# Performance work log

Measured on AMD Instinct MI355X. Metric: run time of the kernel, lower is better.

Reference implementation:

```python
import jax, jax.numpy as jnp
import numpy as np

B, N, C, H = 2, 2048, 1024, 16
D = C // H
SCALE = D ** -0.5


def setup_inputs() -> dict:
    key = jax.random.key(0)
    ks = jax.random.split(key, 5)
    x = jax.random.normal(ks[0], (B, N, C), dtype=jnp.float32)
    # causal mask, broadcast over batch: True = attend
    attention_mask = jnp.broadcast_to(jnp.tril(jnp.ones((N, N), dtype=bool)), (B, N, N))
    w_qkv = jax.random.normal(ks[1], (3 * C, C), dtype=jnp.float32) * (C ** -0.5)
    b_qkv = jax.random.normal(ks[2], (3 * C,), dtype=jnp.float32) * 0.02
    w_proj = jax.random.normal(ks[3], (C, C), dtype=jnp.float32) * (C ** -0.5)
    b_proj = jax.random.normal(ks[4], (C,), dtype=jnp.float32) * 0.02
    return {"x": x, "attention_mask": attention_mask, "w_qkv": w_qkv,
            "b_qkv": b_qkv, "w_proj": w_proj, "b_proj": b_proj}


def reference(x, attention_mask, w_qkv, b_qkv, w_proj, b_proj):
    b, n, c = x.shape
    qkv = x @ w_qkv.T + b_qkv                      # [B,N,3C]
    qkv = qkv.reshape(b, n, 3, H, D).transpose(2, 0, 3, 1, 4)  # [3,B,H,N,D]
    q, k, v = qkv[0], qkv[1], qkv[2]
    dots = jnp.einsum('bhid,bhjd->bhij', q, k) * SCALE
    mask_value = -jnp.finfo(dots.dtype).max
    dots = jnp.where(attention_mask[:, None, :, :], dots, mask_value)
    attn = jax.nn.softmax(dots.astype(jnp.float32), axis=-1).astype(dots.dtype)
    out = jnp.einsum('bhij,bhjd->bhid', attn, v)   # [B,H,N,D]
    # NOTE: original code reshapes WITHOUT transposing heads back - faithful.
    out = out.reshape(b, n, c)
    return out @ w_proj.T + b_proj
```

## Files before the change

kernel.cpp:

```cpp
#include <hip/hip_runtime.h>
#include <hip/hip_bf16.h>
#include <stdint.h>

#define SL_F 0.18033688011112043f

typedef unsigned short u16;
typedef unsigned int u32;
typedef __attribute__((ext_vector_type(8))) short bf16x8;
typedef __attribute__((ext_vector_type(4))) float f32x4;

__device__ __forceinline__ u16 f2bf(float f) {
    union { float f; u32 u; } v; v.f = f;
    return (u16)((v.u + 0x7fffu + ((v.u >> 16) & 1u)) >> 16);
}
__device__ __forceinline__ u32 pack2bf(float a, float b) {
    union { __hip_bfloat162 h; u32 u; } p;
    p.h = __float22bfloat162_rn(make_float2(a, b));
    return p.u;
}

__device__ __forceinline__ void gl_lds16(const u16* g, u16* l) {
    __builtin_amdgcn_global_load_lds(
        (const __attribute__((address_space(1))) u32*)g,
        (__attribute__((address_space(3))) u32*)l, 16, 0, 0);
}

__global__ __launch_bounds__(256) void convert_k(
    const float4* __restrict__ x, const float4* __restrict__ w1,
    const float4* __restrict__ w2,
    ushort4* __restrict__ xb, ushort4* __restrict__ w1b, ushort4* __restrict__ w2b)
{
    const int i = blockIdx.x * 256 + threadIdx.x;
    const int XN = 4096 * 1024 / 4, W1 = 3072 * 1024 / 4;
    float4 v; ushort4* dst;
    if (i < XN)            { v = x[i];            dst = &xb[i]; }
    else if (i < XN + W1)  { v = w1[i - XN];      dst = &w1b[i - XN]; }
    else                   { v = w2[i - XN - W1]; dst = &w2b[i - XN - W1]; }
    ushort4 o;
    o.x = f2bf(v.x); o.y = f2bf(v.y); o.z = f2bf(v.z); o.w = f2bf(v.w);
    *dst = o;
}

__global__ __launch_bounds__(256) void qkv_gemm(
    const u16* __restrict__ A, const u16* __restrict__ Bw,
    const float* __restrict__ bias,
    u16* __restrict__ Qb, u16* __restrict__ Kb, u16* __restrict__ VTb)
{
    __shared__ __align__(16) u16 Al[2][8 * 512];
    __shared__ __align__(16) u16 Bl[2][8 * 512];
    const int tid = threadIdx.x;
    const int lane = tid & 63;
    const int w = tid >> 6;
    const int la = lane & 15, qd = lane >> 4;
    const int K = 1024;
    const int m0 = blockIdx.y * 128;
    const int n0 = blockIdx.x * 128;
    const int wm = (w >> 1) * 64, wn = (w & 1) * 64;

    const u16* Ag0 = A + (size_t)(m0 + (2 * w) * 16 + la) * K + qd * 8;
    const u16* Ag1 = A + (size_t)(m0 + (2 * w + 1) * 16 + la) * K + qd * 8;
    const u16* Bg0 = Bw + (size_t)(n0 + (2 * w) * 16 + la) * K + qd * 8;
    const u16* Bg1 = Bw + (size_t)(n0 + (2 * w + 1) * 16 + la) * K + qd * 8;

    auto stage = [&](int k0, int b) {
        gl_lds16(Ag0 + k0, &Al[b][(2 * w) * 512]);
        gl_lds16(Ag1 + k0, &Al[b][(2 * w + 1) * 512]);
        gl_lds16(Bg0 + k0, &Bl[b][(2 * w) * 512]);
        gl_lds16(Bg1 + k0, &Bl[b][(2 * w + 1) * 512]);
    };

    f32x4 acc[4][4] = {};
    int buf = 0;
    stage(0, 0);

    for (int k0 = 0; k0 < K; k0 += 32) {
        __syncthreads();
        if (k0 + 32 < K) stage(k0 + 32, buf ^ 1);

        bf16x8 af[4], bfr[4];
#pragma unroll
        for (int i = 0; i < 4; i++)
            af[i] = *(const bf16x8*)&Al[buf][(((unsigned)wm >> 4) + i) * 512 + lane * 8];
#pragma unroll
        for (int j = 0; j < 4; j++)
            bfr[j] = *(const bf16x8*)&Bl[buf][(((unsigned)wn >> 4) + j) * 512 + lane * 8];
#pragma unroll
        for (int i = 0; i < 4; i++)
#pragma unroll
            for (int j = 0; j < 4; j++)
                acc[i][j] = __builtin_amdgcn_mfma_f32_16x16x32_bf16(
                    af[i], bfr[j], acc[i][j], 0, 0, 0);
        buf ^= 1;
    }

#pragma unroll
    for (int j = 0; j < 4; j++) {
        const int col = n0 + wn + j * 16 + la;
        const float bv = bias[col];
        const int t = col >> 10, hd = col & 1023, h = hd >> 6, d = hd & 63;
#pragma unroll
        for (int i = 0; i < 4; i++)
#pragma unroll
            for (int r = 0; r < 4; r++) {
                const int row = m0 + wm + i * 16 + qd * 4 + r;
                const int b = row >> 11, n = row & 2047;
                const int bh = b * 16 + h;
                const u16 val = f2bf(acc[i][j][r] + bv);
                if (t == 0)      Qb[((size_t)bh * 2048 + n) * 64 + d] = val;
                else if (t == 1) Kb[((size_t)bh * 2048 + n) * 64 + d] = val;
                else             VTb[((size_t)bh * 64 + d) * 2048 + n] = val;
            }
    }
}

__global__ __launch_bounds__(256) void proj_gemm(
    const u16* __restrict__ A, const u16* __restrict__ Bw,
    const float* __restrict__ bias, float* __restrict__ Out)
{
    __shared__ __align__(16) u16 Al[2][16 * 512];
    __shared__ __align__(16) u16 Bl[2][8 * 512];
    const int tid = threadIdx.x;
    const int lane = tid & 63;
    const int w = tid >> 6;
    const int la = lane & 15, qd = lane >> 4;
    const int K = 1024;
    const int m0 = blockIdx.y * 128;
    const int n0 = blockIdx.x * 64;
    const int wm = (w >> 1) * 64, wn = (w & 1) * 32;

    const u16* Asrc[4];
    const u16* Bsrc[2];
#pragma unroll
    for (int t = 0; t < 4; t++) {
        const int ck = 4 * w + t, g = ck >> 1, h = ck & 1;
        Asrc[t] = A + (size_t)(m0 + g * 16 + la) * K + h * 32 + qd * 8;
    }
#pragma unroll
    for (int t = 0; t < 2; t++) {
        const int ck = 2 * w + t, g = ck >> 1, h = ck & 1;
        Bsrc[t] = Bw + (size_t)(n0 + g * 16 + la) * K + h * 32 + qd * 8;
    }
    auto stage = [&](int k0, int b) {
#pragma unroll
        for (int t = 0; t < 4; t++)
            gl_lds16(Asrc[t] + k0, &Al[b][(4 * w + t) * 512]);
#pragma unroll
        for (int t = 0; t < 2; t++)
            gl_lds16(Bsrc[t] + k0, &Bl[b][(2 * w + t) * 512]);
    };

    f32x4 acc[4][2] = {};
    int buf = 0;
    stage(0, 0);

    for (int k0 = 0; k0 < K; k0 += 64) {
        __syncthreads();
        if (k0 + 64 < K) stage(k0 + 64, buf ^ 1);

        bf16x8 af[4][2], bfr[2][2];
#pragma unroll
        for (int i = 0; i < 4; i++) {
            const int g = ((unsigned)wm >> 4) + i;
#pragma unroll
            for (int h = 0; h < 2; h++)
                af[i][h] = *(const bf16x8*)&Al[buf][(g * 2 + h) * 512 + lane * 8];
        }
#pragma unroll
        for (int j = 0; j < 2; j++) {
            const int g = ((unsigned)wn >> 4) + j;
#pragma unroll
            for (int h = 0; h < 2; h++)
                bfr[j][h] = *(const bf16x8*)&Bl[buf][(g * 2 + h) * 512 + lane * 8];
        }
#pragma unroll
        for (int i = 0; i < 4; i++)
#pragma unroll
            for (int j = 0; j < 2; j++) {
                f32x4 c = acc[i][j];
                c = __builtin_amdgcn_mfma_f32_16x16x32_bf16(af[i][0], bfr[j][0], c, 0, 0, 0);
                c = __builtin_amdgcn_mfma_f32_16x16x32_bf16(af[i][1], bfr[j][1], c, 0, 0, 0);
                acc[i][j] = c;
            }
        buf ^= 1;
    }

#pragma unroll
    for (int j = 0; j < 2; j++) {
        const int col = n0 + wn + j * 16 + la;
        const float bv = bias[col];
#pragma unroll
        for (int i = 0; i < 4; i++)
#pragma unroll
            for (int r = 0; r < 4; r++) {
                const int row = m0 + wm + i * 16 + qd * 4 + r;
                Out[(size_t)row * 1024 + col] = acc[i][j][r] + bv;
            }
    }
}

__global__ __launch_bounds__(256) void attn_k(
    const u16* __restrict__ Qb, const u16* __restrict__ Kb,
    const u16* __restrict__ VTb, u16* __restrict__ Ob)
{
    __shared__ __align__(16) u16 Kl[2][16 * 512];
    __shared__ __align__(16) u16 Vl[2][16 * 512];
    __shared__ __align__(16) u16 Pl[4][16 * 72];
    const int bh = blockIdx.x & 31;
    const int pair = blockIdx.x >> 5;
    const int tid = threadIdx.x;
    const int lane = tid & 63;
    const int w = tid >> 6;
    const int la = lane & 15, qd = lane >> 4;

    const u16* Kbase = Kb + (size_t)bh * 2048 * 64;
    const u16* Vbase = VTb + (size_t)bh * 64 * 2048;
    u16* Pw = &Pl[w][0];

    u32 ksrc[4], vsrc[4];
#pragma unroll
    for (int t = 0; t < 4; t++) {
        const int ck = 4 * w + t;
        ksrc[t] = (u32)((ck >> 1) * 16 + la) * 64 + (ck & 1) * 32 + qd * 8;
        vsrc[t] = (u32)((ck >> 2) * 16 + la) * 2048 + (ck & 3) * 32 + qd * 8;
    }
    auto stage = [&](int j0, int b) {
#pragma unroll
        for (int t = 0; t < 4; t++) {
            gl_lds16(Kbase + (u32)j0 * 64 + ksrc[t], &Kl[b][(4 * w + t) * 512]);
            gl_lds16(Vbase + (u32)j0 + vsrc[t], &Vl[b][(4 * w + t) * 512]);
        }
    };

    int buf = 0;
    stage(0, 0);

    for (int half = 0; half < 2; half++) {
        const int tile = (half == 0) ? pair : 31 - pair;
        const int q0 = tile * 64 + w * 16;
        const int jmax = (tile >> 1) * 128;
        const int qrow = q0 + la;

        const u16* Qp = Qb + ((size_t)bh * 2048 + q0 + la) * 64 + qd * 8;
        const bf16x8 qf0 = *(const bf16x8*)Qp;
        const bf16x8 qf1 = *(const bf16x8*)(Qp + 32);

        f32x4 o[4] = {};
        float lsum = 0.f;

        for (int j0 = 0; j0 <= jmax; j0 += 128) {
            __syncthreads();

            const int nj = (j0 + 128 <= jmax) ? (j0 + 128) : ((half == 0) ? 0 : -1);
            if (nj >= 0) stage(nj, buf ^ 1);

            f32x4 s[8];
#pragma unroll
            for (int c = 0; c < 8; c++) {
                f32x4 z = {};
                const bf16x8 kf0 = *(const bf16x8*)&Kl[buf][(c * 2 + 0) * 512 + lane * 8];
                const bf16x8 kf1 = *(const bf16x8*)&Kl[buf][(c * 2 + 1) * 512 + lane * 8];
                z = __builtin_amdgcn_mfma_f32_16x16x32_bf16(kf0, qf0, z, 0, 0, 0);
                z = __builtin_amdgcn_mfma_f32_16x16x32_bf16(kf1, qf1, z, 0, 0, 0);
                s[c] = z;
            }

            if (j0 == jmax) {
#pragma unroll
                for (int c = 0; c < 8; c++)
#pragma unroll
                    for (int r = 0; r < 4; r++) {
                        const int j = j0 + c * 16 + qd * 4 + r;
                        float v = s[c][r] * SL_F;
                        v = (j > qrow) ? -1e30f : v;
                        s[c][r] = __builtin_amdgcn_exp2f(v);
                    }
            } else {
#pragma unroll
                for (int c = 0; c < 8; c++)
#pragma unroll
                    for (int r = 0; r < 4; r++)
                        s[c][r] = __builtin_amdgcn_exp2f(s[c][r] * SL_F);
            }
#pragma unroll
            for (int c = 0; c < 8; c++)
#pragma unroll
                for (int r = 0; r < 4; r++)
                    lsum += s[c][r];

#pragma unroll
            for (int hh = 0; hh < 2; hh++) {
#pragma unroll
                for (int c = 0; c < 4; c++) {
                    uint2 pw;
                    pw.x = pack2bf(s[hh * 4 + c][0], s[hh * 4 + c][1]);
                    pw.y = pack2bf(s[hh * 4 + c][2], s[hh * 4 + c][3]);
                    *(uint2*)&Pw[la * 72 + c * 16 + qd * 4] = pw;
                }
                const bf16x8 pf0 = *(const bf16x8*)&Pw[la * 72 + qd * 8];
                const bf16x8 pf1 = *(const bf16x8*)&Pw[la * 72 + 32 + qd * 8];
#pragma unroll
                for (int c2 = 0; c2 < 4; c2++) {
                    const bf16x8 vf0 = *(const bf16x8*)&Vl[buf][(c2 * 4 + hh * 2 + 0) * 512 + lane * 8];
                    const bf16x8 vf1 = *(const bf16x8*)&Vl[buf][(c2 * 4 + hh * 2 + 1) * 512 + lane * 8];
                    o[c2] = __builtin_amdgcn_mfma_f32_16x16x32_bf16(pf0, vf0, o[c2], 0, 0, 0);
                    o[c2] = __builtin_amdgcn_mfma_f32_16x16x32_bf16(pf1, vf1, o[c2], 0, 0, 0);
                }
            }
            buf ^= 1;
        }

        lsum += __shfl_xor(lsum, 16, 64);
        lsum += __shfl_xor(lsum, 32, 64);
        float rinv[4];
#pragma unroll
        for (int r = 0; r < 4; r++)
            rinv[r] = 1.0f / __shfl(lsum, qd * 4 + r, 64);

        u16* Op = Ob + (size_t)bh * 2048 * 64;
#pragma unroll
        for (int c2 = 0; c2 < 4; c2++)
#pragma unroll
            for (int r = 0; r < 4; r++) {
                const int row = q0 + qd * 4 + r;
                Op[(size_t)row * 64 + c2 * 16 + la] = f2bf(o[c2][r] * rinv[r]);
            }
    }
}

extern "C" void kernel_launch(void* const* d_in, const int* in_sizes, int n_in,
                              void* d_out, int out_size, void* d_ws, size_t ws_size,
                              hipStream_t stream)
{
    const float* x     = (const float*)d_in[0];
    const float* wqkv  = (const float*)d_in[2];
    const float* bqkv  = (const float*)d_in[3];
    const float* wproj = (const float*)d_in[4];
    const float* bproj = (const float*)d_in[5];
    float* out = (float*)d_out;

    u16* ws     = (u16*)d_ws;
    u16* xb     = ws;
    u16* wqkvb  = xb + 4096 * 1024;
    u16* wprojb = wqkvb + 3072 * 1024;
    u16* Qb     = wprojb + 1024 * 1024;
    u16* Kb     = Qb + 32 * 2048 * 64;
    u16* VTb    = Kb + 32 * 2048 * 64;
    u16* Ob     = VTb + 32 * 2048 * 64;

    convert_k<<<dim3(8192), dim3(256), 0, stream>>>(
        (const float4*)x, (const float4*)wqkv, (const float4*)wproj,
        (ushort4*)xb, (ushort4*)wqkvb, (ushort4*)wprojb);

    qkv_gemm<<<dim3(24, 32), dim3(256), 0, stream>>>(
        xb, wqkvb, bqkv, Qb, Kb, VTb);

    attn_k<<<dim3(512), dim3(256), 0, stream>>>(Qb, Kb, VTb, Ob);

    proj_gemm<<<dim3(16, 32), dim3(256), 0, stream>>>(
        Ob, wprojb, bproj, out);
}
```

Baseline: 228.7 us.

## Pre-swizzle bf16 operands into MFMA fragment layout during conversion

The conversion kernel now writes x, w_qkv and w_proj in a tiled fragment order: 16-row groups by 32-wide k-blocks, each stored as 64 lanes of 8 contiguous bf16. It uses one 16-byte store per thread and half as many threads. qkv_gemm and the proj_gemm B operand now stage each 1 KB fragment with fully contiguous global-to-LDS loads, replacing 16-row strided reads. This is meant to improve global load coalescing in the GEMMs. The trade-off is that the conversion reads are now scattered across rows.

```diff
diff --git a/kernel.cpp b/kernel.cpp
--- a/kernel.cpp
+++ b/kernel.cpp
@@ -26,19 +26,28 @@
 }
 
 __global__ __launch_bounds__(256) void convert_k(
-    const float4* __restrict__ x, const float4* __restrict__ w1,
-    const float4* __restrict__ w2,
-    ushort4* __restrict__ xb, ushort4* __restrict__ w1b, ushort4* __restrict__ w2b)
-{
-    const int i = blockIdx.x * 256 + threadIdx.x;
-    const int XN = 4096 * 1024 / 4, W1 = 3072 * 1024 / 4;
-    float4 v; ushort4* dst;
-    if (i < XN)            { v = x[i];            dst = &xb[i]; }
-    else if (i < XN + W1)  { v = w1[i - XN];      dst = &w1b[i - XN]; }
-    else                   { v = w2[i - XN - W1]; dst = &w2b[i - XN - W1]; }
-    ushort4 o;
-    o.x = f2bf(v.x); o.y = f2bf(v.y); o.z = f2bf(v.z); o.w = f2bf(v.w);
-    *dst = o;
+    const float* __restrict__ x, const float* __restrict__ w1,
+    const float* __restrict__ w2,
+    u16* __restrict__ xb, u16* __restrict__ w1b, u16* __restrict__ w2b)
+{
+    const int t = blockIdx.x * 256 + threadIdx.x;
+    const int XA = 524288, XW1 = 393216;
+    const float* src; u16* dst; int s;
+    if (t < XA)            { src = x;  dst = xb;  s = t; }
+    else if (t < XA + XW1) { src = w1; dst = w1b; s = t - XA; }
+    else                   { src = w2; dst = w2b; s = t - XA - XW1; }
+    const int c = s >> 6;
+    const int u = s & 63;
+    const int l = (u >> 2) + 16 * (u & 3);
+    const int g = c >> 5, kb = c & 31;
+    const int row = g * 16 + (l & 15);
+    const int k0 = kb * 32 + (l >> 4) * 8;
+    const float4 v0 = *(const float4*)&src[(size_t)row * 1024 + k0];
+    const float4 v1 = *(const float4*)&src[(size_t)row * 1024 + k0 + 4];
+    uint4 o;
+    o.x = pack2bf(v0.x, v0.y); o.y = pack2bf(v0.z, v0.w);
+    o.z = pack2bf(v1.x, v1.y); o.w = pack2bf(v1.z, v1.w);
+    *(uint4*)&dst[((size_t)c * 64 + l) * 8] = o;
 }
 
 __global__ __launch_bounds__(256) void qkv_gemm(
@@ -52,30 +61,30 @@
     const int lane = tid & 63;
     const int w = tid >> 6;
     const int la = lane & 15, qd = lane >> 4;
-    const int K = 1024;
     const int m0 = blockIdx.y * 128;
     const int n0 = blockIdx.x * 128;
     const int wm = (w >> 1) * 64, wn = (w & 1) * 64;
 
-    const u16* Ag0 = A + (size_t)(m0 + (2 * w) * 16 + la) * K + qd * 8;
-    const u16* Ag1 = A + (size_t)(m0 + (2 * w + 1) * 16 + la) * K + qd * 8;
-    const u16* Bg0 = Bw + (size_t)(n0 + (2 * w) * 16 + la) * K + qd * 8;
-    const u16* Bg1 = Bw + (size_t)(n0 + (2 * w + 1) * 16 + la) * K + qd * 8;
+    const u16* Ag0 = A + ((size_t)((m0 >> 4) + 2 * w) * 32) * 512 + lane * 8;
+    const u16* Ag1 = Ag0 + 32 * 512;
+    const u16* Bg0 = Bw + ((size_t)((n0 >> 4) + 2 * w) * 32) * 512 + lane * 8;
+    const u16* Bg1 = Bg0 + 32 * 512;
 
     auto stage = [&](int k0, int b) {
-        gl_lds16(Ag0 + k0, &Al[b][(2 * w) * 512]);
-        gl_lds16(Ag1 + k0, &Al[b][(2 * w + 1) * 512]);
-        gl_lds16(Bg0 + k0, &Bl[b][(2 * w) * 512]);
-        gl_lds16(Bg1 + k0, &Bl[b][(2 * w + 1) * 512]);
+        const size_t ko = (size_t)(k0 >> 5) * 512;
+        gl_lds16(Ag0 + ko, &Al[b][(2 * w) * 512]);
+        gl_lds16(Ag1 + ko, &Al[b][(2 * w + 1) * 512]);
+        gl_lds16(Bg0 + ko, &Bl[b][(2 * w) * 512]);
+        gl_lds16(Bg1 + ko, &Bl[b][(2 * w + 1) * 512]);
     };
 
     f32x4 acc[4][4] = {};
     int buf = 0;
     stage(0, 0);
 
-    for (int k0 = 0; k0 < K; k0 += 32) {
+    for (int k0 = 0; k0 < 1024; k0 += 32) {
         __syncthreads();
-        if (k0 + 32 < K) stage(k0 + 32, buf ^ 1);
+        if (k0 + 32 < 1024) stage(k0 + 32, buf ^ 1);
 
         bf16x8 af[4], bfr[4];
 #pragma unroll
@@ -129,24 +138,20 @@
     const int wm = (w >> 1) * 64, wn = (w & 1) * 32;
 
     const u16* Asrc[4];
-    const u16* Bsrc[2];
 #pragma unroll
     for (int t = 0; t < 4; t++) {
         const int ck = 4 * w + t, g = ck >> 1, h = ck & 1;
         Asrc[t] = A + (size_t)(m0 + g * 16 + la) * K + h * 32 + qd * 8;
     }
-#pragma unroll
-    for (int t = 0; t < 2; t++) {
-        const int ck = 2 * w + t, g = ck >> 1, h = ck & 1;
-        Bsrc[t] = Bw + (size_t)(n0 + g * 16 + la) * K + h * 32 + qd * 8;
-    }
+    const u16* Bg = Bw + ((size_t)((n0 >> 4) + w) * 32) * 512 + lane * 8;
+
     auto stage = [&](int k0, int b) {
 #pragma unroll
         for (int t = 0; t < 4; t++)
             gl_lds16(Asrc[t] + k0, &Al[b][(4 * w + t) * 512]);
 #pragma unroll
         for (int t = 0; t < 2; t++)
-            gl_lds16(Bsrc[t] + k0, &Bl[b][(2 * w + t) * 512]);
+            gl_lds16(Bg + (size_t)((k0 >> 5) + t) * 512, &Bl[b][(2 * w + t) * 512]);
     };
 
     f32x4 acc[4][2] = {};
@@ -347,9 +352,8 @@
     u16* VTb    = Kb + 32 * 2048 * 64;
     u16* Ob     = VTb + 32 * 2048 * 64;
 
-    convert_k<<<dim3(8192), dim3(256), 0, stream>>>(
-        (const float4*)x, (const float4*)wqkv, (const float4*)wproj,
-        (ushort4*)xb, (ushort4*)wqkvb, (ushort4*)wprojb);
+    convert_k<<<dim3(4096), dim3(256), 0, stream>>>(
+        x, wqkv, wproj, xb, wqkvb, wprojb);
 
     qkv_gemm<<<dim3(24, 32), dim3(256), 0, stream>>>(
         xb, wqkvb, bqkv, Qb, Kb, VTb);
```

Result: faster. 209.2 us (-8.5%).
